# Kernel optimization log

Measured on AMD Instinct MI355X. Metric: run time of the kernel, lower is better.

The kernel has to match this reference:

```python
import jax, jax.numpy as jnp
import numpy as np

B, L, D = 8, 2048, 1024
LN_EPS = 1e-5
WKV_EPS = 1e-8


def _ln(x, g, b):
    m = x.mean(-1, keepdims=True)
    v = x.var(-1, keepdims=True)  # biased var, matches torch LayerNorm
    return (x - m) * jax.lax.rsqrt(v + LN_EPS) * g + b


def _shift(x):
    # ZeroPad2d((0,0,1,-1)): x_prev[:, t] = x[:, t-1], x_prev[:, 0] = 0
    return jnp.pad(x, ((0, 0), (1, 0), (0, 0)))[:, :-1]


def _wkv(k, v, time_decay, time_first):
    # Faithful to the torch loop: t=0 uses exp(u + k0); t>0 decays prior state
    # (including the u-boosted first term) by exp(-exp(time_decay)).
    ew = jnp.exp(-jnp.exp(time_decay))  # [D]
    e0 = jnp.exp(time_first + k[:, 0])  # [B, D]
    a0 = e0 * v[:, 0]
    b0 = e0

    def step(carry, kv):
        a, b = carry
        kt, vt = kv
        ek = jnp.exp(kt)
        a = ew * a + ek * vt
        b = ew * b + ek
        return (a, b), a / (b + WKV_EPS)

    xs = (jnp.swapaxes(k[:, 1:], 0, 1), jnp.swapaxes(v[:, 1:], 0, 1))  # [L-1, B, D]
    _, outs = jax.lax.scan(step, (a0, b0), xs)
    out0 = (a0 / (b0 + WKV_EPS))[:, None]  # [B, 1, D]
    return jnp.concatenate([out0, jnp.swapaxes(outs, 0, 1)], axis=1)  # [B, L, D]


def setup_inputs() -> dict:
    key = jax.random.key(0)
    ks = jax.random.split(key, 10)
    s = 1.0 / np.sqrt(D)

    def w(k, shape, scale):
        return jax.random.normal(k, shape, jnp.float32) * scale

    return {
        "x": jax.random.normal(ks[0], (B, L, D), jnp.float32),
        "ln1_g": jnp.ones((D,), jnp.float32),
        "ln1_b": jnp.zeros((D,), jnp.float32),
        "Wk": w(ks[1], (D, D), s),
        "Wv": w(ks[2], (D, D), s),
        "Wr": w(ks[3], (D, D), s),
        "Wo": w(ks[4], (D, D), s),
        "time_decay": w(ks[5], (D,), 0.1),
        "time_first": w(ks[6], (D,), 0.1),
        "mix_k": jnp.full((D,), 0.5, jnp.float32),
        "mix_v": jnp.full((D,), 0.5, jnp.float32),
        "mix_r": jnp.full((D,), 0.5, jnp.float32),
        "ln2_g": jnp.ones((D,), jnp.float32),
        "ln2_b": jnp.zeros((D,), jnp.float32),
        "Wfk": w(ks[7], (D, 4 * D), s),
        "Wfv": w(ks[8], (4 * D, D), 1.0 / np.sqrt(4 * D)),
        "Wfr": w(ks[9], (D, D), s),
    }


def reference(x, ln1_g, ln1_b, Wk, Wv, Wr, Wo, time_decay, time_first,
              mix_k, mix_v, mix_r, ln2_g, ln2_b, Wfk, Wfv, Wfr):
    # --- time mixing ---
    xn = _ln(x, ln1_g, ln1_b)
    xp = _shift(xn)
    k = (xn * mix_k + xp * (1.0 - mix_k)) @ Wk
    v = (xn * mix_v + xp * (1.0 - mix_v)) @ Wv
    r = jax.nn.sigmoid((xn * mix_r + xp * (1.0 - mix_r)) @ Wr)
    wkv = _wkv(k, v, time_decay, time_first)
    x = x + (r * wkv) @ Wo
    # --- channel mixing ---
    yn = _ln(x, ln2_g, ln2_b)
    yp = _shift(yn)
    kk = jnp.square(jax.nn.relu((0.5 * yn + 0.5 * yp) @ Wfk))
    rr = jax.nn.sigmoid(yn @ Wfr)
    return x + rr * (kk @ Wfv)
```

## Files before the change

### kernel.cpp

```cpp
#include <hip/hip_runtime.h>
#include <hip/hip_bf16.h>
#include <stdint.h>

typedef __hip_bfloat16 bf16_t;
typedef __attribute__((ext_vector_type(8))) short bf16x8;
typedef __attribute__((ext_vector_type(4))) float f32x4;

#define DEV static __device__ __forceinline__

constexpr int kBB = 8, kL = 2048, kD = 1024;
constexpr int kM = kBB * kL;
constexpr int kSeg = 32, kP = 64;

DEV float bf2f(unsigned short u) { return __uint_as_float((unsigned)u << 16); }
DEV unsigned short f2bf(float f) {
  unsigned u = __float_as_uint(f);
  return (unsigned short)((u + 0x7fffu + ((u >> 16) & 1u)) >> 16);
}

DEV void gld16(const void* g, void* l) {
  const __attribute__((address_space(1))) unsigned* gp =
      (const __attribute__((address_space(1))) unsigned*)(uintptr_t)g;
  __attribute__((address_space(3))) unsigned* lp =
      (__attribute__((address_space(3))) unsigned*)(unsigned)(uintptr_t)l;
  __builtin_amdgcn_global_load_lds(gp, lp, 16, 0, 0);
}

__global__ __launch_bounds__(256) void k_transpose_cast(
    const float* __restrict__ W, bf16_t* __restrict__ Wt, int R, int C) {
  __shared__ float tile[32][33];
  const int bx = blockIdx.x * 32;
  const int by = blockIdx.y * 32;
  const int tx = threadIdx.x & 31, ty = threadIdx.x >> 5;
#pragma unroll
  for (int i = 0; i < 32; i += 8)
    tile[ty + i][tx] = W[(size_t)(by + ty + i) * C + (bx + tx)];
  __syncthreads();
#pragma unroll
  for (int i = 0; i < 32; i += 8)
    Wt[(size_t)(bx + ty + i) * R + (by + tx)] = __float2bfloat16(tile[tx][ty + i]);
}

__global__ __launch_bounds__(256) void k_ln_stats(
    const float* __restrict__ X, float* __restrict__ mean, float* __restrict__ rstd) {
  const int row = blockIdx.x * 4 + (threadIdx.x >> 6);
  const int lane = threadIdx.x & 63;
  const float4* xr = (const float4*)(X + (size_t)row * kD);
  float s = 0.f, s2 = 0.f;
#pragma unroll
  for (int i = 0; i < 4; ++i) {
    float4 v = xr[lane + 64 * i];
    s += v.x + v.y + v.z + v.w;
    s2 += v.x * v.x + v.y * v.y + v.z * v.z + v.w * v.w;
  }
#pragma unroll
  for (int off = 32; off > 0; off >>= 1) {
    s += __shfl_xor(s, off);
    s2 += __shfl_xor(s2, off);
  }
  if (lane == 0) {
    float m = s * (1.f / kD);
    float var = fmaxf(s2 * (1.f / kD) - m * m, 0.f);
    mean[row] = m;
    rstd[row] = rsqrtf(var + 1e-5f);
  }
}

__global__ __launch_bounds__(256) void k_ln_mix1(
    const float* __restrict__ X, const float* __restrict__ mean, const float* __restrict__ rstd,
    const float* __restrict__ g, const float* __restrict__ be,
    const float* __restrict__ mk, const float* __restrict__ mv, const float* __restrict__ mr,
    bf16_t* __restrict__ ok, bf16_t* __restrict__ ov, bf16_t* __restrict__ orr) {
  const int row = blockIdx.x;
  const int l = row & (kL - 1);
  const int i = threadIdx.x;
  const bool hp = (l != 0);
  const float m0 = mean[row], s0 = rstd[row];
  const float m1 = hp ? mean[row - 1] : 0.f;
  const float s1 = hp ? rstd[row - 1] : 0.f;
  float xa[4], pa[4] = {0.f, 0.f, 0.f, 0.f}, ga[4], ba[4], ka[4], va[4], ra[4];
  *(float4*)xa = ((const float4*)(X + (size_t)row * kD))[i];
  if (hp) *(float4*)pa = ((const float4*)(X + (size_t)(row - 1) * kD))[i];
  *(float4*)ga = ((const float4*)g)[i];
  *(float4*)ba = ((const float4*)be)[i];
  *(float4*)ka = ((const float4*)mk)[i];
  *(float4*)va = ((const float4*)mv)[i];
  *(float4*)ra = ((const float4*)mr)[i];
  ushort4 uk, uv, ur;
  unsigned short* pk = (unsigned short*)&uk;
  unsigned short* pv = (unsigned short*)&uv;
  unsigned short* pr = (unsigned short*)&ur;
#pragma unroll
  for (int c = 0; c < 4; ++c) {
    float xn = (xa[c] - m0) * s0 * ga[c] + ba[c];
    float xp = hp ? (pa[c] - m1) * s1 * ga[c] + ba[c] : 0.f;
    pk[c] = f2bf(xn * ka[c] + xp * (1.f - ka[c]));
    pv[c] = f2bf(xn * va[c] + xp * (1.f - va[c]));
    pr[c] = f2bf(xn * ra[c] + xp * (1.f - ra[c]));
  }
  ((ushort4*)(ok + (size_t)row * kD))[i] = uk;
  ((ushort4*)(ov + (size_t)row * kD))[i] = uv;
  ((ushort4*)(orr + (size_t)row * kD))[i] = ur;
}

__global__ __launch_bounds__(256) void k_ln_mix2(
    const float* __restrict__ X, const float* __restrict__ mean, const float* __restrict__ rstd,
    const float* __restrict__ g, const float* __restrict__ be,
    bf16_t* __restrict__ om, bf16_t* __restrict__ on) {
  const int row = blockIdx.x;
  const int l = row & (kL - 1);
  const int i = threadIdx.x;
  const bool hp = (l != 0);
  const float m0 = mean[row], s0 = rstd[row];
  const float m1 = hp ? mean[row - 1] : 0.f;
  const float s1 = hp ? rstd[row - 1] : 0.f;
  float xa[4], pa[4] = {0.f, 0.f, 0.f, 0.f}, ga[4], ba[4];
  *(float4*)xa = ((const float4*)(X + (size_t)row * kD))[i];
  if (hp) *(float4*)pa = ((const float4*)(X + (size_t)(row - 1) * kD))[i];
  *(float4*)ga = ((const float4*)g)[i];
  *(float4*)ba = ((const float4*)be)[i];
  ushort4 um, un;
  unsigned short* qm = (unsigned short*)&um;
  unsigned short* qn = (unsigned short*)&un;
#pragma unroll
  for (int c = 0; c < 4; ++c) {
    float yn = (xa[c] - m0) * s0 * ga[c] + ba[c];
    float yp = hp ? (pa[c] - m1) * s1 * ga[c] + ba[c] : 0.f;
    qm[c] = f2bf(0.5f * (yn + yp));
    qn[c] = f2bf(yn);
  }
  ((ushort4*)(om + (size_t)row * kD))[i] = um;
  ((ushort4*)(on + (size_t)row * kD))[i] = un;
}

__global__ __launch_bounds__(256) void k_wkv_seg(
    const unsigned short* __restrict__ kq, const unsigned short* __restrict__ vq,
    const float* __restrict__ td, const float* __restrict__ tf,
    float* __restrict__ segA, float* __restrict__ segB) {
  const int d = blockIdx.x * 256 + threadIdx.x;
  const int b = blockIdx.y;
  const int s = blockIdx.z;
  const float ew = __expf(-__expf(td[d]));
  const float uu = (s == 0) ? tf[d] : 0.f;
  const size_t base = ((size_t)b * kL + (size_t)s * kP) * kD + d;
  float a = 0.f, bb = 0.f;
  unsigned short kA[16], vA[16], kB[16], vB[16];
  auto pref = [&](unsigned short* ka, unsigned short* va, int c) {
    const size_t o0 = base + (size_t)c * 16 * kD;
#pragma unroll
    for (int j = 0; j < 16; ++j) {
      ka[j] = kq[o0 + (size_t)j * kD];
      va[j] = vq[o0 + (size_t)j * kD];
    }
  };
  auto comp = [&](const unsigned short* ka, const unsigned short* va, int c) {
#pragma unroll
    for (int j = 0; j < 16; ++j) {
      float kf = bf2f(ka[j]);
      if (s == 0 && c == 0 && j == 0) kf += uu;
      float ek = __expf(kf);
      a = ew * a + ek * bf2f(va[j]);
      bb = ew * bb + ek;
    }
  };
  pref(kA, vA, 0);
  pref(kB, vB, 1); comp(kA, vA, 0);
  pref(kA, vA, 2); comp(kB, vB, 1);
  pref(kB, vB, 3); comp(kA, vA, 2);
  comp(kB, vB, 3);
  const size_t sidx = ((size_t)b * kSeg + s) * kD + d;
  segA[sidx] = a;
  segB[sidx] = bb;
}

__global__ __launch_bounds__(256) void k_wkv_carry(
    const float* __restrict__ td,
    const float* __restrict__ segA, const float* __restrict__ segB,
    float* __restrict__ carA, float* __restrict__ carB) {
  const int d = blockIdx.x * 256 + threadIdx.x;
  const int b = blockIdx.y;
  const float ew = __expf(-__expf(td[d]));
  float ewP = ew;
#pragma unroll
  for (int i = 0; i < 6; ++i) ewP *= ewP;
  float ca = 0.f, cb = 0.f;
#pragma unroll 4
  for (int s = 0; s < kSeg; ++s) {
    const size_t idx = ((size_t)b * kSeg + s) * kD + d;
    carA[idx] = ca;
    carB[idx] = cb;
    ca = ewP * ca + segA[idx];
    cb = ewP * cb + segB[idx];
  }
}

__global__ __launch_bounds__(256) void k_wkv_out(
    const unsigned short* __restrict__ kq, const unsigned short* __restrict__ vq,
    const unsigned short* __restrict__ rq, const float* __restrict__ td,
    const float* __restrict__ tf, const float* __restrict__ carA,
    const float* __restrict__ carB, unsigned short* __restrict__ out) {
  const int d = blockIdx.x * 256 + threadIdx.x;
  const int b = blockIdx.y;
  const int s = blockIdx.z;
  const float ew = __expf(-__expf(td[d]));
  const float uu = (s == 0) ? tf[d] : 0.f;
  const size_t base = ((size_t)b * kL + (size_t)s * kP) * kD + d;
  const size_t sidx = ((size_t)b * kSeg + s) * kD + d;
  float a = carA[sidx], bb = carB[sidx];
  unsigned short kA[16], vA[16], rA[16], kB[16], vB[16], rB[16];
  auto pref = [&](unsigned short* ka, unsigned short* va, unsigned short* ra, int c) {
    const size_t o0 = base + (size_t)c * 16 * kD;
#pragma unroll
    for (int j = 0; j < 16; ++j) {
      ka[j] = kq[o0 + (size_t)j * kD];
      va[j] = vq[o0 + (size_t)j * kD];
      ra[j] = rq[o0 + (size_t)j * kD];
    }
  };
  auto comp = [&](const unsigned short* ka, const unsigned short* va,
                  const unsigned short* ra, int c) {
    const size_t o0 = base + (size_t)c * 16 * kD;
#pragma unroll
    for (int j = 0; j < 16; ++j) {
      float kf = bf2f(ka[j]);
      if (s == 0 && c == 0 && j == 0) kf += uu;
      float ek = __expf(kf);
      a = ew * a + ek * bf2f(va[j]);
      bb = ew * bb + ek;
      float y = a / (bb + 1e-8f);
      float sr = 1.f / (1.f + __expf(-bf2f(ra[j])));
      out[o0 + (size_t)j * kD] = f2bf(sr * y);
    }
  };
  pref(kA, vA, rA, 0);
  pref(kB, vB, rB, 1); comp(kA, vA, rA, 0);
  pref(kA, vA, rA, 2); comp(kB, vB, rB, 1);
  pref(kB, vB, rB, 3); comp(kA, vA, rA, 2);
  comp(kB, vB, rB, 3);
}

template <int EPI>
__global__ __launch_bounds__(512) void gemm256(
    const bf16_t* __restrict__ A0, long strA, int lda,
    const bf16_t* __restrict__ B0, long strB, int ldb,
    bf16_t* __restrict__ Cb0, float* __restrict__ Cf, long strC,
    int N, int K, int nbx,
    const float* __restrict__ addf, const bf16_t* __restrict__ mulb) {
  __shared__ __align__(16) char lds[98304];
  const int z = blockIdx.z;
  const bf16_t* A = A0 + (size_t)z * strA;
  const bf16_t* Bt = B0 + (size_t)z * strB;
  const int nwg = gridDim.x;
  const int wg = (blockIdx.x & 7) * (nwg >> 3) + (blockIdx.x >> 3);
  const int by = wg / nbx, bx = wg - by * nbx;
  const long brow = (long)by * 128;
  const long bcol = (long)bx * 256;
  const int tid = threadIdx.x;
  const int lane = tid & 63;
  const int wr = (tid >> 6) >> 2, wc = (tid >> 6) & 3;

  f32x4 acc[4][4] = {};

  const int trow = tid >> 3;
  const int scol = ((tid & 7) * 16) ^ ((trow & 7) << 4);
  const char* As0 = (const char*)(A + (brow + trow) * (size_t)lda) + scol;
  const char* As1 = As0 + 64L * lda * 2;
  const char* Bs0 = (const char*)(Bt + (bcol + trow) * (size_t)ldb) + scol;
  const char* Bs1 = Bs0 + 64L * ldb * 2;
  const char* Bs2 = Bs0 + 128L * ldb * 2;
  const char* Bs3 = Bs0 + 192L * ldb * 2;
  char* Ad = lds + tid * 16;
  char* Bd = lds + 32768 + tid * 16;

#define STAGE(kt, p)                                    \
  {                                                     \
    const long kb = (long)(kt) * 128;                   \
    gld16(As0 + kb, Ad + (p) * 16384);                  \
    gld16(As1 + kb, Ad + (p) * 16384 + 8192);           \
    gld16(Bs0 + kb, Bd + (p) * 32768);                  \
    gld16(Bs1 + kb, Bd + (p) * 32768 + 8192);           \
    gld16(Bs2 + kb, Bd + (p) * 32768 + 16384);          \
    gld16(Bs3 + kb, Bd + (p) * 32768 + 24576);          \
  }

  const int l16 = lane & 15, kq = lane >> 4;
  const int swz = (l16 & 7) << 4;
  const int o0 = (kq * 16) ^ swz;
  const int o1 = (64 + kq * 16) ^ swz;
  const char* Ar = lds + (wr * 64 + l16) * 128;
  const char* Br = lds + 32768 + (wc * 64 + l16) * 128;

  const int NT = K >> 6;
  STAGE(0, 0)
  STAGE(1, 1)
  asm volatile("s_waitcnt vmcnt(6)" ::: "memory");
  __builtin_amdgcn_s_barrier();

  for (int t = 0; t < NT; ++t) {
    const int p = t & 1;
    const char* Ap = Ar + p * 16384;
    const char* Bp = Br + p * 32768;
    bf16x8 af[4][2], bf[4][2];
#pragma unroll
    for (int m = 0; m < 4; ++m) {
      af[m][0] = *(const bf16x8*)(Ap + m * 2048 + o0);
      af[m][1] = *(const bf16x8*)(Ap + m * 2048 + o1);
    }
#pragma unroll
    for (int n = 0; n < 4; ++n) {
      bf[n][0] = *(const bf16x8*)(Bp + n * 2048 + o0);
      bf[n][1] = *(const bf16x8*)(Bp + n * 2048 + o1);
    }
    asm volatile("s_waitcnt lgkmcnt(0)" ::: "memory");
    __builtin_amdgcn_sched_barrier(0);
    __builtin_amdgcn_s_barrier();
    const bool st = (t + 2 < NT);
    if (st) STAGE(t + 2, p)
    __builtin_amdgcn_s_setprio(1);
#pragma unroll
    for (int m = 0; m < 4; ++m)
#pragma unroll
      for (int n = 0; n < 4; ++n) {
        acc[m][n] = __builtin_amdgcn_mfma_f32_16x16x32_bf16(af[m][0], bf[n][0], acc[m][n], 0, 0, 0);
        acc[m][n] = __builtin_amdgcn_mfma_f32_16x16x32_bf16(af[m][1], bf[n][1], acc[m][n], 0, 0, 0);
      }
    __builtin_amdgcn_s_setprio(0);
    if (t + 1 < NT) {
      if (st) asm volatile("s_waitcnt vmcnt(6)" ::: "memory");
      else    asm volatile("s_waitcnt vmcnt(0)" ::: "memory");
      __builtin_amdgcn_s_barrier();
    }
  }
#undef STAGE

  bf16_t* Cb = Cb0 + (size_t)z * strC;
  const long orow = brow + wr * 64 + (lane >> 4) * 4;
  const long ocol = bcol + wc * 64 + l16;
#pragma unroll
  for (int m = 0; m < 4; ++m) {
#pragma unroll
    for (int reg = 0; reg < 4; ++reg) {
      const long r = orow + m * 16 + reg;
#pragma unroll
      for (int n = 0; n < 4; ++n) {
        const size_t idx = (size_t)r * N + ocol + n * 16;
        const float v = acc[m][n][reg];
        if constexpr (EPI == 0) {
          Cb[idx] = __float2bfloat16(v);
        } else if constexpr (EPI == 1) {
          Cf[idx] = addf[idx] + v;
        } else if constexpr (EPI == 2) {
          float u = v > 0.f ? v : 0.f;
          Cb[idx] = __float2bfloat16(u * u);
        } else if constexpr (EPI == 3) {
          Cb[idx] = __float2bfloat16(1.f / (1.f + __expf(-v)));
        } else if constexpr (EPI == 4) {
          Cf[idx] = v;
        } else {
          Cf[idx] = addf[idx] + __bfloat162float(mulb[idx]) * (Cf[idx] + v);
        }
      }
    }
  }
}

extern "C" void kernel_launch(void* const* d_in, const int* in_sizes, int n_in,
                              void* d_out, int out_size, void* d_ws, size_t ws_size,
                              hipStream_t stream) {
  const float* x    = (const float*)d_in[0];
  const float* ln1g = (const float*)d_in[1];
  const float* ln1b = (const float*)d_in[2];
  const float* Wk   = (const float*)d_in[3];
  const float* Wv   = (const float*)d_in[4];
  const float* Wr   = (const float*)d_in[5];
  const float* Wo   = (const float*)d_in[6];
  const float* td   = (const float*)d_in[7];
  const float* tf   = (const float*)d_in[8];
  const float* mk   = (const float*)d_in[9];
  const float* mv   = (const float*)d_in[10];
  const float* mr   = (const float*)d_in[11];
  const float* ln2g = (const float*)d_in[12];
  const float* ln2b = (const float*)d_in[13];
  const float* Wfk  = (const float*)d_in[14];
  const float* Wfv  = (const float*)d_in[15];
  const float* Wfr  = (const float*)d_in[16];

  char* ws = (char*)d_ws;
  const size_t MB = 1ull << 20;
  bf16_t* WkT  = (bf16_t*)(ws + 0 * MB);
  bf16_t* WvT  = (bf16_t*)(ws + 2 * MB);
  bf16_t* WrT  = (bf16_t*)(ws + 4 * MB);
  bf16_t* WoT  = (bf16_t*)(ws + 6 * MB);
  bf16_t* WfkT = (bf16_t*)(ws + 8 * MB);
  bf16_t* WfvT = (bf16_t*)(ws + 16 * MB);
  bf16_t* WfrT = (bf16_t*)(ws + 24 * MB);
  float* mean1 = (float*)(ws + 26 * MB);
  float* rstd1 = (float*)(ws + 26 * MB + 65536);
  float* mean2 = (float*)(ws + 26 * MB + 131072);
  float* rstd2 = (float*)(ws + 26 * MB + 196608);
  bf16_t* xk   = (bf16_t*)(ws + 28 * MB);
  bf16_t* xv   = (bf16_t*)(ws + 60 * MB);
  bf16_t* xr   = (bf16_t*)(ws + 92 * MB);
  bf16_t* kbuf = (bf16_t*)(ws + 124 * MB);
  bf16_t* vbuf = (bf16_t*)(ws + 156 * MB);
  bf16_t* rbuf = (bf16_t*)(ws + 188 * MB);
  float*  segA = (float*)(ws + 60 * MB);
  float*  segB = (float*)(ws + 61 * MB);
  float*  carA = (float*)(ws + 62 * MB);
  float*  carB = (float*)(ws + 63 * MB);
  bf16_t* rwkv = (bf16_t*)(ws + 92 * MB);
  float*  x1   = (float*)(ws + 28 * MB);
  bf16_t* rr   = (bf16_t*)(ws + 92 * MB);
  bf16_t* ynb  = (bf16_t*)(ws + 124 * MB);
  bf16_t* kk   = (bf16_t*)(ws + 124 * MB);
  bf16_t* ymix = (bf16_t*)(ws + 188 * MB);
  float*  out  = (float*)d_out;
  const long sX = (long)kM * kD;
  const long sW = (long)kD * kD;

  dim3 blk(256), blkg(512);
  k_transpose_cast<<<dim3(32, 32), blk, 0, stream>>>(Wk, WkT, 1024, 1024);
  k_transpose_cast<<<dim3(32, 32), blk, 0, stream>>>(Wv, WvT, 1024, 1024);
  k_transpose_cast<<<dim3(32, 32), blk, 0, stream>>>(Wr, WrT, 1024, 1024);
  k_transpose_cast<<<dim3(32, 32), blk, 0, stream>>>(Wo, WoT, 1024, 1024);
  k_transpose_cast<<<dim3(128, 32), blk, 0, stream>>>(Wfk, WfkT, 1024, 4096);
  k_transpose_cast<<<dim3(32, 128), blk, 0, stream>>>(Wfv, WfvT, 4096, 1024);
  k_transpose_cast<<<dim3(32, 32), blk, 0, stream>>>(Wfr, WfrT, 1024, 1024);

  k_ln_stats<<<kM / 4, blk, 0, stream>>>(x, mean1, rstd1);
  k_ln_mix1<<<kM, blk, 0, stream>>>(x, mean1, rstd1, ln1g, ln1b, mk, mv, mr, xk, xv, xr);
  gemm256<0><<<dim3(512, 1, 3), blkg, 0, stream>>>(xk, sX, 1024, WkT, sW, 1024,
      kbuf, nullptr, sX, 1024, 1024, 4, nullptr, nullptr);
  k_wkv_seg<<<dim3(4, 8, kSeg), blk, 0, stream>>>((const unsigned short*)kbuf,
      (const unsigned short*)vbuf, td, tf, segA, segB);
  k_wkv_carry<<<dim3(4, 8), blk, 0, stream>>>(td, segA, segB, carA, carB);
  k_wkv_out<<<dim3(4, 8, kSeg), blk, 0, stream>>>((const unsigned short*)kbuf,
      (const unsigned short*)vbuf, (const unsigned short*)rbuf, td, tf, carA, carB,
      (unsigned short*)rwkv);
  gemm256<1><<<512, blkg, 0, stream>>>(rwkv, 0, 1024, WoT, 0, 1024,
      nullptr, x1, 0, 1024, 1024, 4, x, nullptr);

  k_ln_stats<<<kM / 4, blk, 0, stream>>>(x1, mean2, rstd2);
  k_ln_mix2<<<kM, blk, 0, stream>>>(x1, mean2, rstd2, ln2g, ln2b, ymix, ynb);
  gemm256<3><<<512, blkg, 0, stream>>>(ynb, 0, 1024, WfrT, 0, 1024,
      rr, nullptr, 0, 1024, 1024, 4, nullptr, nullptr);
  for (int c = 0; c < 2; ++c) {
    gemm256<2><<<1024, blkg, 0, stream>>>(ymix, 0, 1024, WfkT + (size_t)c * 2048 * 1024, 0, 1024,
        kk, nullptr, 0, 2048, 1024, 8, nullptr, nullptr);
    if (c == 0)
      gemm256<4><<<512, blkg, 0, stream>>>(kk, 0, 2048, WfvT + 0, 0, 4096,
          nullptr, out, 0, 1024, 2048, 4, nullptr, nullptr);
    else
      gemm256<6><<<512, blkg, 0, stream>>>(kk, 0, 2048, WfvT + 2048, 0, 4096,
          nullptr, out, 0, 1024, 2048, 4, x1, rr);
  }
}
```

Before: 756.7 us.

## Triple-buffer GEMM LDS stages and prefetch K-half fragments into registers

Replaces the double-buffered LDS pipeline in the GEMM kernel with three stages, so two tiles are in flight from global memory at a time. Each K tile is split into even and odd halves, and the register fragments for the next tile's first half are loaded while the current tile's second half runs. This removes one barrier per iteration and is meant to overlap LDS reads with MFMA work. In exchange LDS use grows to 144KB, and the new launch bound of two blocks per CU caps the register budget, which risks spilling given the accumulators plus four fragment sets.

```diff
diff --git a/kernel.cpp b/kernel.cpp
--- a/kernel.cpp
+++ b/kernel.cpp
@@ -240,13 +240,13 @@
 }
 
 template <int EPI>
-__global__ __launch_bounds__(512) void gemm256(
+__global__ __launch_bounds__(512, 2) void gemm256(
     const bf16_t* __restrict__ A0, long strA, int lda,
     const bf16_t* __restrict__ B0, long strB, int ldb,
     bf16_t* __restrict__ Cb0, float* __restrict__ Cf, long strC,
     int N, int K, int nbx,
     const float* __restrict__ addf, const bf16_t* __restrict__ mulb) {
-  __shared__ __align__(16) char lds[98304];
+  __shared__ __align__(16) char lds[147456];
   const int z = blockIdx.z;
   const bf16_t* A = A0 + (size_t)z * strA;
   const bf16_t* Bt = B0 + (size_t)z * strB;
@@ -269,67 +269,82 @@
   const char* Bs1 = Bs0 + 64L * ldb * 2;
   const char* Bs2 = Bs0 + 128L * ldb * 2;
   const char* Bs3 = Bs0 + 192L * ldb * 2;
-  char* Ad = lds + tid * 16;
-  char* Bd = lds + 32768 + tid * 16;
-
-#define STAGE(kt, p)                                    \
-  {                                                     \
-    const long kb = (long)(kt) * 128;                   \
-    gld16(As0 + kb, Ad + (p) * 16384);                  \
-    gld16(As1 + kb, Ad + (p) * 16384 + 8192);           \
-    gld16(Bs0 + kb, Bd + (p) * 32768);                  \
-    gld16(Bs1 + kb, Bd + (p) * 32768 + 8192);           \
-    gld16(Bs2 + kb, Bd + (p) * 32768 + 16384);          \
-    gld16(Bs3 + kb, Bd + (p) * 32768 + 24576);          \
+
+#define STAGE(kt, p)                                   \
+  {                                                    \
+    const long kb = (long)(kt) * 128;                  \
+    char* Ad = lds + (p) * 49152 + tid * 16;           \
+    char* Bd = Ad + 16384;                             \
+    gld16(As0 + kb, Ad);                               \
+    gld16(As1 + kb, Ad + 8192);                        \
+    gld16(Bs0 + kb, Bd);                               \
+    gld16(Bs1 + kb, Bd + 8192);                        \
+    gld16(Bs2 + kb, Bd + 16384);                       \
+    gld16(Bs3 + kb, Bd + 24576);                       \
   }
 
   const int l16 = lane & 15, kq = lane >> 4;
   const int swz = (l16 & 7) << 4;
-  const int o0 = (kq * 16) ^ swz;
-  const int o1 = (64 + kq * 16) ^ swz;
-  const char* Ar = lds + (wr * 64 + l16) * 128;
-  const char* Br = lds + 32768 + (wc * 64 + l16) * 128;
-
+  const int oS0 = (kq * 16) ^ swz;
+  const int oS1 = (64 + kq * 16) ^ swz;
+  const int arow = (wr * 64 + l16) * 128;
+  const int brl = 16384 + (wc * 64 + l16) * 128;
+
+  bf16x8 aE[4], bE[4], aO[4], bO[4];
   const int NT = K >> 6;
-  STAGE(0, 0)
-  STAGE(1, 1)
-  asm volatile("s_waitcnt vmcnt(6)" ::: "memory");
+
+  STAGE(0, 0) STAGE(1, 1) STAGE(2, 2)
+  asm volatile("s_waitcnt vmcnt(12)" ::: "memory");
   __builtin_amdgcn_s_barrier();
-
+  {
+    const char* Ar = lds + arow;
+    const char* Br = lds + brl;
+#pragma unroll
+    for (int m = 0; m < 4; ++m) aE[m] = *(const bf16x8*)(Ar + m * 2048 + oS0);
+#pragma unroll
+    for (int n = 0; n < 4; ++n) bE[n] = *(const bf16x8*)(Br + n * 2048 + oS0);
+  }
+
+  int cur = 0;
   for (int t = 0; t < NT; ++t) {
-    const int p = t & 1;
-    const char* Ap = Ar + p * 16384;
-    const char* Bp = Br + p * 32768;
-    bf16x8 af[4][2], bf[4][2];
-#pragma unroll
-    for (int m = 0; m < 4; ++m) {
-      af[m][0] = *(const bf16x8*)(Ap + m * 2048 + o0);
-      af[m][1] = *(const bf16x8*)(Ap + m * 2048 + o1);
-    }
-#pragma unroll
-    for (int n = 0; n < 4; ++n) {
-      bf[n][0] = *(const bf16x8*)(Bp + n * 2048 + o0);
-      bf[n][1] = *(const bf16x8*)(Bp + n * 2048 + o1);
-    }
+    const int nxt = (cur < 2) ? cur + 1 : 0;
+    const char* Ac = lds + cur * 49152 + arow;
+    const char* Bc = lds + cur * 49152 + brl - 16384 + 16384;
+#pragma unroll
+    for (int m = 0; m < 4; ++m) aO[m] = *(const bf16x8*)(Ac + m * 2048 + oS1);
+#pragma unroll
+    for (int n = 0; n < 4; ++n) bO[n] = *(const bf16x8*)(Bc + n * 2048 + oS1);
+    __builtin_amdgcn_s_setprio(1);
+#pragma unroll
+    for (int m = 0; m < 4; ++m)
+#pragma unroll
+      for (int n = 0; n < 4; ++n)
+        acc[m][n] = __builtin_amdgcn_mfma_f32_16x16x32_bf16(aE[m], bE[n], acc[m][n], 0, 0, 0);
+    __builtin_amdgcn_s_setprio(0);
     asm volatile("s_waitcnt lgkmcnt(0)" ::: "memory");
-    __builtin_amdgcn_sched_barrier(0);
+    if (t + 2 < NT) {
+      asm volatile("s_waitcnt vmcnt(6)" ::: "memory");
+    } else {
+      asm volatile("s_waitcnt vmcnt(0)" ::: "memory");
+    }
     __builtin_amdgcn_s_barrier();
-    const bool st = (t + 2 < NT);
-    if (st) STAGE(t + 2, p)
+    if (t + 3 < NT) STAGE(t + 3, cur)
+    if (t + 1 < NT) {
+      const char* An = lds + nxt * 49152 + arow;
+      const char* Bn = lds + nxt * 49152 + brl;
+#pragma unroll
+      for (int m = 0; m < 4; ++m) aE[m] = *(const bf16x8*)(An + m * 2048 + oS0);
+#pragma unroll
+      for (int n = 0; n < 4; ++n) bE[n] = *(const bf16x8*)(Bn + n * 2048 + oS0);
+    }
     __builtin_amdgcn_s_setprio(1);
 #pragma unroll
     for (int m = 0; m < 4; ++m)
 #pragma unroll
-      for (int n = 0; n < 4; ++n) {
-        acc[m][n] = __builtin_amdgcn_mfma_f32_16x16x32_bf16(af[m][0], bf[n][0], acc[m][n], 0, 0, 0);
-        acc[m][n] = __builtin_amdgcn_mfma_f32_16x16x32_bf16(af[m][1], bf[n][1], acc[m][n], 0, 0, 0);
-      }
+      for (int n = 0; n < 4; ++n)
+        acc[m][n] = __builtin_amdgcn_mfma_f32_16x16x32_bf16(aO[m], bO[n], acc[m][n], 0, 0, 0);
     __builtin_amdgcn_s_setprio(0);
-    if (t + 1 < NT) {
-      if (st) asm volatile("s_waitcnt vmcnt(6)" ::: "memory");
-      else    asm volatile("s_waitcnt vmcnt(0)" ::: "memory");
-      __builtin_amdgcn_s_barrier();
-    }
+    cur = nxt;
   }
 #undef STAGE
 
```

Result: faster. 728.3 us (-3.8%).
